# Optimization experiments

Measured on AMD Instinct MI355X. Metric: run time of the kernel, lower is better.

Reference implementation:

```python
import jax, jax.numpy as jnp
import numpy as np

N, FIN, H, FOUT = 4096, 128, 4, 64
NEG_INF = -1e9


def _xavier(key, shape):
    fan_in, fan_out = shape[-2], shape[-1]
    limit = float(np.sqrt(6.0 / (fan_in + fan_out)))
    return jax.random.uniform(key, shape, jnp.float32, -limit, limit)


def setup_inputs() -> dict:
    key = jax.random.key(0)
    ks = jax.random.split(key, 7)
    x = jax.random.normal(ks[0], (N, FIN), jnp.float32)
    u = jax.random.uniform(ks[1], (N, N))
    mask = jnp.where(u < 0.02, 0.0, NEG_INF).astype(jnp.float32)
    idx = jnp.arange(N)
    mask = mask.at[idx, idx].set(0.0)
    proj_param = _xavier(ks[2], (H, FIN, FOUT))          # per-head projection
    score_src = _xavier(ks[3], (H, FOUT, 1))             # scoring_fn_source (IMP1 layout)
    score_tgt = _xavier(ks[4], (H, FOUT, 1))             # scoring_fn_target
    skip_w = _xavier(ks[5], (H * FOUT, FIN))             # skip_proj Linear weight
    bias = jnp.zeros((H * FOUT,), jnp.float32)
    return {"x": x, "mask": mask, "proj_param": proj_param,
            "score_src": score_src, "score_tgt": score_tgt,
            "skip_w": skip_w, "bias": bias}


def reference(x, mask, proj_param, score_src, score_tgt, skip_w, bias):
    # project: [1,N,Fin] @ [H,Fin,Fout] -> [H,N,Fout]
    h = jnp.einsum('nf,hfo->hno', x, proj_param)
    # additive (Bahdanau-style) scores
    s_src = jnp.matmul(h, score_src)                     # [H,N,1]
    s_tgt = jnp.matmul(h, score_tgt)                     # [H,N,1]
    all_scores = jax.nn.leaky_relu(s_src + jnp.swapaxes(s_tgt, 1, 2), 0.2)  # [H,N,N]
    attn = jax.nn.softmax(all_scores + mask[None, :, :], axis=-1)           # [H,N,N]
    # aggregate: [H,N,N] @ [H,N,Fout] -> [N,H,Fout]
    out = jnp.einsum('hnm,hmo->nho', attn, h)
    # skip connection (dims differ: Fin != H*Fout -> use skip_proj)
    out = out + jnp.matmul(x, skip_w.T).reshape(N, H, FOUT)
    out = out.reshape(N, H * FOUT) + bias                # concat heads + bias
    return jax.nn.elu(out)
```

## Files before the change

kernel.cpp:

```cpp
#include <hip/hip_runtime.h>
#include <hip/hip_bf16.h>
#include <math.h>


#define NN   4096
#define FIN  128
#define NH   4
#define FO   64
#define HF   256
#define SEG  96
#define LIST 192

typedef unsigned short ushort_t;
typedef unsigned int uint4n __attribute__((ext_vector_type(4)));

__device__ __forceinline__ ushort_t f2bf(float f) {
    __hip_bfloat16 h = __float2bfloat16(f);
    union { __hip_bfloat16 h; ushort_t u; } c; c.h = h; return c.u;
}
__device__ __forceinline__ float bf2f(ushort_t u) {
    union { unsigned int i; float f; } c; c.i = ((unsigned int)u) << 16; return c.f;
}

__global__ __launch_bounds__(256) void k1_gemm(
        const float* __restrict__ x,
        const float* __restrict__ proj,
        const float* __restrict__ skw,
        const float* __restrict__ asrc,
        const float* __restrict__ atgt,
        ushort_t* __restrict__ h2b, float* __restrict__ skip_ws,
        float* __restrict__ src4, float* __restrict__ tgt4) {
    __shared__ float sA[64 * 132];
    __shared__ float sB[128 * 64];
    const int tid = threadIdx.x;
    const int bc  = blockIdx.x;
    const int i0  = blockIdx.y * 64;

    {
        const float4* src = (const float4*)(x + (size_t)i0 * FIN);
        #pragma unroll
        for (int q = 0; q < 8; q++) {
            int s   = tid + q * 256;
            int row = s >> 5;
            int c4  = (s & 31) << 2;
            float4 v = src[s];
            float* d = sA + row * 132 + c4;
            d[0] = v.x; d[1] = v.y; d[2] = v.z; d[3] = v.w;
        }
    }
    if (bc < 4) {
        const float4* src = (const float4*)(proj + (size_t)bc * FIN * FO);
        #pragma unroll
        for (int q = 0; q < 8; q++) {
            int s = tid + q * 256;
            *(float4*)(sB + (size_t)s * 4) = src[s];
        }
    } else {
        const float* sw = skw + (size_t)(bc - 4) * 64 * FIN;
        #pragma unroll
        for (int q = 0; q < 8; q++) {
            int s  = tid + q * 256;
            int c  = s & 63;
            int k4 = (s >> 6) << 2;
            float4 v = *(const float4*)(sw + (size_t)c * FIN + k4);
            sB[(k4 + 0) * 64 + c] = v.x;
            sB[(k4 + 1) * 64 + c] = v.y;
            sB[(k4 + 2) * 64 + c] = v.z;
            sB[(k4 + 3) * 64 + c] = v.w;
        }
    }
    __syncthreads();

    const int tx = tid & 15, ty = tid >> 4;
    const int r0 = ty << 2, c0 = tx << 2;
    float acc[4][4] = {};
    #pragma unroll 2
    for (int k = 0; k < FIN; k += 4) {
        alignas(16) float a[4][4];
        alignas(16) float b[4][4];
        #pragma unroll
        for (int rr = 0; rr < 4; rr++)
            *(float4*)a[rr] = *(const float4*)(sA + (r0 + rr) * 132 + k);
        #pragma unroll
        for (int kk = 0; kk < 4; kk++)
            *(float4*)b[kk] = *(const float4*)(sB + (k + kk) * 64 + c0);
        #pragma unroll
        for (int kk = 0; kk < 4; kk++)
            #pragma unroll
            for (int rr = 0; rr < 4; rr++)
                #pragma unroll
                for (int cc = 0; cc < 4; cc++)
                    acc[rr][cc] = fmaf(a[rr][kk], b[kk][cc], acc[rr][cc]);
    }

    if (bc < 4) {
        #pragma unroll
        for (int rr = 0; rr < 4; rr++) {
            ushort4 hv;
            hv.x = f2bf(acc[rr][0]); hv.y = f2bf(acc[rr][1]);
            hv.z = f2bf(acc[rr][2]); hv.w = f2bf(acc[rr][3]);
            *(ushort4*)(h2b + (size_t)(i0 + r0 + rr) * HF + bc * 64 + c0) = hv;
        }
        float as[4], at[4];
        #pragma unroll
        for (int cc = 0; cc < 4; cc++) {
            as[cc] = asrc[bc * FO + c0 + cc];
            at[cc] = atgt[bc * FO + c0 + cc];
        }
        #pragma unroll
        for (int rr = 0; rr < 4; rr++) {
            float ps = acc[rr][0] * as[0] + acc[rr][1] * as[1]
                     + acc[rr][2] * as[2] + acc[rr][3] * as[3];
            float pt = acc[rr][0] * at[0] + acc[rr][1] * at[1]
                     + acc[rr][2] * at[2] + acc[rr][3] * at[3];
            #pragma unroll
            for (int off = 8; off >= 1; off >>= 1) {
                ps += __shfl_xor(ps, off, 64);
                pt += __shfl_xor(pt, off, 64);
            }
            if (tx == 0) {
                int i = i0 + r0 + rr;
                src4[(size_t)i * 4 + bc] = ps;
                tgt4[(size_t)i * 4 + bc] = pt;
            }
        }
    } else {
        float* dst = skip_ws + (size_t)i0 * HF + (bc - 4) * 64;
        #pragma unroll
        for (int rr = 0; rr < 4; rr++)
            *(float4*)(dst + (size_t)(r0 + rr) * HF + c0) = *(float4*)acc[rr];
    }
}

__global__ __launch_bounds__(256) void k2a_scan(
        const unsigned int* __restrict__ mask,
        ushort_t* __restrict__ list,
        int* __restrict__ cnt) {
    __shared__ ushort_t s_nbr[4 * SEG];
    __shared__ int s_wt[4];
    const int tid  = threadIdx.x;
    const int lane = tid & 63, w = tid >> 6;
    const int i    = blockIdx.x;

    const uint4n* mrow = (const uint4n*)(mask + (size_t)i * NN);
    uint4n mv[4];
    #pragma unroll
    for (int s = 0; s < 4; s++)
        mv[s] = __builtin_nontemporal_load(&mrow[w * 256 + s * 64 + lane]);

    int base = 0;
    #pragma unroll
    for (int s = 0; s < 4; s++) {
        #pragma unroll
        for (int e = 0; e < 4; e++) {
            bool hit = (mv[s][e] & 0x7fffffffu) == 0u;
            unsigned long long bal = __ballot(hit);
            int pre = __builtin_amdgcn_mbcnt_hi(
                          (unsigned int)(bal >> 32),
                          __builtin_amdgcn_mbcnt_lo((unsigned int)bal, 0));
            if (hit) {
                int slot = base + pre;
                if (slot < SEG)
                    s_nbr[w * SEG + slot] =
                        (ushort_t)(w * 1024 + s * 256 + lane * 4 + e);
            }
            base += (int)__popcll(bal);
        }
    }
    if (lane == 0) s_wt[w] = base < SEG ? base : SEG;
    __syncthreads();

    const int t0 = s_wt[0], t1 = s_wt[1], t2 = s_wt[2], t3 = s_wt[3];
    const int off = (w > 0 ? t0 : 0) + (w > 1 ? t1 : 0) + (w > 2 ? t2 : 0);
    const int mine = s_wt[w];
    ushort_t* dst = list + (size_t)i * LIST;
    for (int kk = lane; kk < mine; kk += 64) {
        int p = off + kk;
        if (p < LIST) dst[p] = s_nbr[w * SEG + kk];
    }
    if (tid == 0) {
        int tot = t0 + t1 + t2 + t3;
        cnt[i] = tot < LIST ? tot : LIST;
    }
}

__global__ __launch_bounds__(256) void k2b_attn(
        const ushort_t* __restrict__ list,
        const int* __restrict__ cnt,
        const ushort_t* __restrict__ h2b,
        const float* __restrict__ skip_ws,
        const float* __restrict__ src4,
        const float* __restrict__ tgt4,
        const float* __restrict__ bias,
        float* __restrict__ out) {
    __shared__ float s_p[4][LIST];
    __shared__ int   s_j[LIST];
    const int tid  = threadIdx.x;
    const int lane = tid & 63, w = tid >> 6;
    const int i    = blockIdx.x;
    const int col  = w * 64 + lane;

    const float skipv = skip_ws[(size_t)i * HF + col];
    const float bv    = bias[col];
    const float sc    = src4[(size_t)i * 4 + w];
    int c = cnt[i];
    c = c < LIST ? c : LIST;

    const ushort_t* lp = list + (size_t)i * LIST;
    for (int kk = tid; kk < c; kk += 256) s_j[kk] = lp[kk];
    __syncthreads();

    float lsum = 0.f;
    for (int kk = lane; kk < c; kk += 64) {
        int j = s_j[kk];
        float p = sc + tgt4[(size_t)j * 4 + w];
        p = p > 0.f ? p : 0.2f * p;
        p = __expf(p);
        s_p[w][kk] = p;
        lsum += p;
    }
    #pragma unroll
    for (int off = 32; off >= 1; off >>= 1)
        lsum += __shfl_xor(lsum, off, 64);
    const float inv = lsum > 0.f ? 1.0f / lsum : 0.0f;

    const ushort_t* hp = h2b + col;
    const float* ps = s_p[w];
    float acc = 0.f;
    int kk = 0;
    for (; kk + 8 <= c; kk += 8) {
        int j0 = s_j[kk + 0], j1 = s_j[kk + 1], j2 = s_j[kk + 2], j3 = s_j[kk + 3];
        int j4 = s_j[kk + 4], j5 = s_j[kk + 5], j6 = s_j[kk + 6], j7 = s_j[kk + 7];
        float p0 = ps[kk + 0], p1 = ps[kk + 1], p2 = ps[kk + 2], p3 = ps[kk + 3];
        float p4 = ps[kk + 4], p5 = ps[kk + 5], p6 = ps[kk + 6], p7 = ps[kk + 7];
        float h0 = bf2f(hp[(size_t)j0 * HF]);
        float h1 = bf2f(hp[(size_t)j1 * HF]);
        float h2v = bf2f(hp[(size_t)j2 * HF]);
        float h3 = bf2f(hp[(size_t)j3 * HF]);
        float h4 = bf2f(hp[(size_t)j4 * HF]);
        float h5 = bf2f(hp[(size_t)j5 * HF]);
        float h6 = bf2f(hp[(size_t)j6 * HF]);
        float h7 = bf2f(hp[(size_t)j7 * HF]);
        acc = fmaf(p0, h0, acc);  acc = fmaf(p1, h1, acc);
        acc = fmaf(p2, h2v, acc); acc = fmaf(p3, h3, acc);
        acc = fmaf(p4, h4, acc);  acc = fmaf(p5, h5, acc);
        acc = fmaf(p6, h6, acc);  acc = fmaf(p7, h7, acc);
    }
    for (; kk < c; kk++)
        acc = fmaf(ps[kk], bf2f(hp[(size_t)s_j[kk] * HF]), acc);

    float vv = acc * inv + skipv + bv;
    vv = vv > 0.f ? vv : expm1f(vv);
    out[(size_t)i * HF + col] = vv;
}

extern "C" void kernel_launch(void* const* d_in, const int* in_sizes, int n_in,
                              void* d_out, int out_size, void* d_ws, size_t ws_size,
                              hipStream_t stream) {
    const float*        x    = (const float*)d_in[0];
    const unsigned int* mask = (const unsigned int*)d_in[1];
    const float*        proj = (const float*)d_in[2];
    const float*        asrc = (const float*)d_in[3];
    const float*        atgt = (const float*)d_in[4];
    const float*        skw  = (const float*)d_in[5];
    const float*        bias = (const float*)d_in[6];
    float*              out  = (float*)d_out;

    char* ws = (char*)d_ws;
    ushort_t* h2b     = (ushort_t*)ws;
    float*    skip_ws = (float*)(ws + (2u << 20));
    float*    src4    = (float*)(ws + (6u << 20));
    float*    tgt4    = (float*)(ws + (6u << 20) + (64u << 10));
    ushort_t* list    = (ushort_t*)(ws + (8u << 20));
    int*      cntp    = (int*)(ws + (10u << 20));

    hipLaunchKernelGGL(k2a_scan, dim3(4096), dim3(256), 0, stream,
                       mask, list, cntp);
    hipLaunchKernelGGL(k1_gemm, dim3(8, 64), dim3(256), 0, stream,
                       x, proj, skw, asrc, atgt, h2b, skip_ws, src4, tgt4);
    hipLaunchKernelGGL(k2b_attn, dim3(4096), dim3(256), 0, stream,
                       list, cntp, h2b, skip_ws, src4, tgt4, bias, out);
}
```

Measured before the change: 144.6 us.

## Fuse mask scan and projection GEMM into one launch with K-split tiles

Merges the mask-scan kernel and the projection/skip GEMM kernel into one launch. The first 512 blocks do the GEMM and the remaining 4096 blocks scan mask rows. The GEMM now stages K in two 64-wide chunks, which halves its shared-memory footprint to about 34 KB so more blocks fit per CU. This removes one kernel launch and lets the small GEMM overlap with the bandwidth-bound mask scan. The cost is an extra barrier in the GEMM and block-divergent role dispatch inside one kernel.

```diff
diff --git a/kernel.cpp b/kernel.cpp
--- a/kernel.cpp
+++ b/kernel.cpp
@@ -10,6 +10,7 @@
 #define HF   256
 #define SEG  96
 #define LIST 192
+#define GEMM_BLOCKS 512
 
 typedef unsigned short ushort_t;
 typedef unsigned int uint4n __attribute__((ext_vector_type(4)));
@@ -22,75 +23,130 @@
     union { unsigned int i; float f; } c; c.i = ((unsigned int)u) << 16; return c.f;
 }
 
-__global__ __launch_bounds__(256) void k1_gemm(
+__global__ __launch_bounds__(256) void k0_fused(
         const float* __restrict__ x,
         const float* __restrict__ proj,
         const float* __restrict__ skw,
         const float* __restrict__ asrc,
         const float* __restrict__ atgt,
+        const unsigned int* __restrict__ mask,
         ushort_t* __restrict__ h2b, float* __restrict__ skip_ws,
-        float* __restrict__ src4, float* __restrict__ tgt4) {
-    __shared__ float sA[64 * 132];
-    __shared__ float sB[128 * 64];
+        float* __restrict__ src4, float* __restrict__ tgt4,
+        ushort_t* __restrict__ list, int* __restrict__ cnt) {
+    __shared__ float sA[64 * 68];
+    __shared__ float sB[64 * 64];
     const int tid = threadIdx.x;
-    const int bc  = blockIdx.x;
-    const int i0  = blockIdx.y * 64;
-
-    {
-        const float4* src = (const float4*)(x + (size_t)i0 * FIN);
-        #pragma unroll
-        for (int q = 0; q < 8; q++) {
-            int s   = tid + q * 256;
-            int row = s >> 5;
-            int c4  = (s & 31) << 2;
-            float4 v = src[s];
-            float* d = sA + row * 132 + c4;
-            d[0] = v.x; d[1] = v.y; d[2] = v.z; d[3] = v.w;
-        }
-    }
-    if (bc < 4) {
-        const float4* src = (const float4*)(proj + (size_t)bc * FIN * FO);
-        #pragma unroll
-        for (int q = 0; q < 8; q++) {
-            int s = tid + q * 256;
-            *(float4*)(sB + (size_t)s * 4) = src[s];
-        }
-    } else {
-        const float* sw = skw + (size_t)(bc - 4) * 64 * FIN;
-        #pragma unroll
-        for (int q = 0; q < 8; q++) {
-            int s  = tid + q * 256;
-            int c  = s & 63;
-            int k4 = (s >> 6) << 2;
-            float4 v = *(const float4*)(sw + (size_t)c * FIN + k4);
-            sB[(k4 + 0) * 64 + c] = v.x;
-            sB[(k4 + 1) * 64 + c] = v.y;
-            sB[(k4 + 2) * 64 + c] = v.z;
-            sB[(k4 + 3) * 64 + c] = v.w;
-        }
-    }
-    __syncthreads();
-
+    const int blk = blockIdx.x;
+
+    if (blk >= GEMM_BLOCKS) {
+        const int i    = blk - GEMM_BLOCKS;
+        ushort_t* s_nbr = (ushort_t*)sA;
+        int*      s_wt  = (int*)sB;
+        const int lane = tid & 63, w = tid >> 6;
+
+        const uint4n* mrow = (const uint4n*)(mask + (size_t)i * NN);
+        uint4n mv[4];
+        #pragma unroll
+        for (int s = 0; s < 4; s++)
+            mv[s] = __builtin_nontemporal_load(&mrow[w * 256 + s * 64 + lane]);
+
+        int base = 0;
+        #pragma unroll
+        for (int s = 0; s < 4; s++) {
+            #pragma unroll
+            for (int e = 0; e < 4; e++) {
+                bool hit = (mv[s][e] & 0x7fffffffu) == 0u;
+                unsigned long long bal = __ballot(hit);
+                int pre = __builtin_amdgcn_mbcnt_hi(
+                              (unsigned int)(bal >> 32),
+                              __builtin_amdgcn_mbcnt_lo((unsigned int)bal, 0));
+                if (hit) {
+                    int slot = base + pre;
+                    if (slot < SEG)
+                        s_nbr[w * SEG + slot] =
+                            (ushort_t)(w * 1024 + s * 256 + lane * 4 + e);
+                }
+                base += (int)__popcll(bal);
+            }
+        }
+        if (lane == 0) s_wt[w] = base < SEG ? base : SEG;
+        __syncthreads();
+
+        const int t0 = s_wt[0], t1 = s_wt[1], t2 = s_wt[2], t3 = s_wt[3];
+        const int off = (w > 0 ? t0 : 0) + (w > 1 ? t1 : 0) + (w > 2 ? t2 : 0);
+        const int mine = s_wt[w];
+        ushort_t* dst = list + (size_t)i * LIST;
+        for (int kk = lane; kk < mine; kk += 64) {
+            int p = off + kk;
+            if (p < LIST) dst[p] = s_nbr[w * SEG + kk];
+        }
+        if (tid == 0) {
+            int tot = t0 + t1 + t2 + t3;
+            cnt[i] = tot < LIST ? tot : LIST;
+        }
+        return;
+    }
+
+    const int bc = blk >> 6;
+    const int i0 = (blk & 63) * 64;
     const int tx = tid & 15, ty = tid >> 4;
     const int r0 = ty << 2, c0 = tx << 2;
     float acc[4][4] = {};
-    #pragma unroll 2
-    for (int k = 0; k < FIN; k += 4) {
-        alignas(16) float a[4][4];
-        alignas(16) float b[4][4];
-        #pragma unroll
-        for (int rr = 0; rr < 4; rr++)
-            *(float4*)a[rr] = *(const float4*)(sA + (r0 + rr) * 132 + k);
-        #pragma unroll
-        for (int kk = 0; kk < 4; kk++)
-            *(float4*)b[kk] = *(const float4*)(sB + (k + kk) * 64 + c0);
-        #pragma unroll
-        for (int kk = 0; kk < 4; kk++)
+
+    #pragma unroll
+    for (int kb = 0; kb < FIN; kb += 64) {
+        if (kb) __syncthreads();
+        #pragma unroll
+        for (int q = 0; q < 4; q++) {
+            int s   = tid + q * 256;
+            int row = s >> 4;
+            int c4  = (s & 15) << 2;
+            float4 v = *(const float4*)(x + (size_t)(i0 + row) * FIN + kb + c4);
+            float* d = sA + row * 68 + c4;
+            d[0] = v.x; d[1] = v.y; d[2] = v.z; d[3] = v.w;
+        }
+        if (bc < 4) {
+            const float4* src = (const float4*)(proj + (size_t)bc * FIN * FO
+                                                + (size_t)kb * FO);
+            #pragma unroll
+            for (int q = 0; q < 4; q++) {
+                int s = tid + q * 256;
+                *(float4*)(sB + (size_t)s * 4) = src[s];
+            }
+        } else {
+            const float* sw = skw + (size_t)(bc - 4) * 64 * FIN;
+            #pragma unroll
+            for (int q = 0; q < 4; q++) {
+                int s  = tid + q * 256;
+                int c  = s & 63;
+                int k4 = (s >> 6) << 2;
+                float4 v = *(const float4*)(sw + (size_t)c * FIN + kb + k4);
+                sB[(k4 + 0) * 64 + c] = v.x;
+                sB[(k4 + 1) * 64 + c] = v.y;
+                sB[(k4 + 2) * 64 + c] = v.z;
+                sB[(k4 + 3) * 64 + c] = v.w;
+            }
+        }
+        __syncthreads();
+
+        #pragma unroll 2
+        for (int k = 0; k < 64; k += 4) {
+            alignas(16) float a[4][4];
+            alignas(16) float b[4][4];
             #pragma unroll
             for (int rr = 0; rr < 4; rr++)
+                *(float4*)a[rr] = *(const float4*)(sA + (r0 + rr) * 68 + k);
+            #pragma unroll
+            for (int kk = 0; kk < 4; kk++)
+                *(float4*)b[kk] = *(const float4*)(sB + (k + kk) * 64 + c0);
+            #pragma unroll
+            for (int kk = 0; kk < 4; kk++)
                 #pragma unroll
-                for (int cc = 0; cc < 4; cc++)
-                    acc[rr][cc] = fmaf(a[rr][kk], b[kk][cc], acc[rr][cc]);
+                for (int rr = 0; rr < 4; rr++)
+                    #pragma unroll
+                    for (int cc = 0; cc < 4; cc++)
+                        acc[rr][cc] = fmaf(a[rr][kk], b[kk][cc], acc[rr][cc]);
+        }
     }
 
     if (bc < 4) {
@@ -129,58 +185,6 @@
         #pragma unroll
         for (int rr = 0; rr < 4; rr++)
             *(float4*)(dst + (size_t)(r0 + rr) * HF + c0) = *(float4*)acc[rr];
-    }
-}
-
-__global__ __launch_bounds__(256) void k2a_scan(
-        const unsigned int* __restrict__ mask,
-        ushort_t* __restrict__ list,
-        int* __restrict__ cnt) {
-    __shared__ ushort_t s_nbr[4 * SEG];
-    __shared__ int s_wt[4];
-    const int tid  = threadIdx.x;
-    const int lane = tid & 63, w = tid >> 6;
-    const int i    = blockIdx.x;
-
-    const uint4n* mrow = (const uint4n*)(mask + (size_t)i * NN);
-    uint4n mv[4];
-    #pragma unroll
-    for (int s = 0; s < 4; s++)
-        mv[s] = __builtin_nontemporal_load(&mrow[w * 256 + s * 64 + lane]);
-
-    int base = 0;
-    #pragma unroll
-    for (int s = 0; s < 4; s++) {
-        #pragma unroll
-        for (int e = 0; e < 4; e++) {
-            bool hit = (mv[s][e] & 0x7fffffffu) == 0u;
-            unsigned long long bal = __ballot(hit);
-            int pre = __builtin_amdgcn_mbcnt_hi(
-                          (unsigned int)(bal >> 32),
-                          __builtin_amdgcn_mbcnt_lo((unsigned int)bal, 0));
-            if (hit) {
-                int slot = base + pre;
-                if (slot < SEG)
-                    s_nbr[w * SEG + slot] =
-                        (ushort_t)(w * 1024 + s * 256 + lane * 4 + e);
-            }
-            base += (int)__popcll(bal);
-        }
-    }
-    if (lane == 0) s_wt[w] = base < SEG ? base : SEG;
-    __syncthreads();
-
-    const int t0 = s_wt[0], t1 = s_wt[1], t2 = s_wt[2], t3 = s_wt[3];
-    const int off = (w > 0 ? t0 : 0) + (w > 1 ? t1 : 0) + (w > 2 ? t2 : 0);
-    const int mine = s_wt[w];
-    ushort_t* dst = list + (size_t)i * LIST;
-    for (int kk = lane; kk < mine; kk += 64) {
-        int p = off + kk;
-        if (p < LIST) dst[p] = s_nbr[w * SEG + kk];
-    }
-    if (tid == 0) {
-        int tot = t0 + t1 + t2 + t3;
-        cnt[i] = tot < LIST ? tot : LIST;
     }
 }
 
@@ -274,10 +278,9 @@
     ushort_t* list    = (ushort_t*)(ws + (8u << 20));
     int*      cntp    = (int*)(ws + (10u << 20));
 
-    hipLaunchKernelGGL(k2a_scan, dim3(4096), dim3(256), 0, stream,
-                       mask, list, cntp);
-    hipLaunchKernelGGL(k1_gemm, dim3(8, 64), dim3(256), 0, stream,
-                       x, proj, skw, asrc, atgt, h2b, skip_ws, src4, tgt4);
-    hipLaunchKernelGGL(k2b_attn, dim3(4096), dim3(256), 0, stream,
+    hipLaunchKernelGGL(k0_fused, dim3(GEMM_BLOCKS + NN), dim3(256), 0, stream,
+                       x, proj, skw, asrc, atgt, mask,
+                       h2b, skip_ws, src4, tgt4, list, cntp);
+    hipLaunchKernelGGL(k2b_attn, dim3(NN), dim3(256), 0, stream,
                        list, cntp, h2b, skip_ws, src4, tgt4, bias, out);
 }
```

Result: faster. 140.1 us (-3.1%).
